# Kernel tuning notes

Measured on AMD Instinct MI355X. Metric: run time of the kernel, lower is better.

Reference implementation:

```python
import jax, jax.numpy as jnp
import numpy as np

N_NODES = 100000
N_EDGES = 1600000
IN_C, HID_C, OUT_C = 128, 128, 128


def setup_inputs() -> dict:
    key = jax.random.key(0)
    k_x, k_e, k_w1, k_w2 = jax.random.split(key, 4)
    x = jax.random.normal(k_x, (N_NODES, IN_C), dtype=jnp.float32)
    edge_index = jax.random.randint(k_e, (2, N_EDGES), 0, N_NODES, dtype=jnp.int64)
    # Glorot-style init for GCNConv linear weights
    s1 = (6.0 / (IN_C + HID_C)) ** 0.5
    s2 = (6.0 / (HID_C + OUT_C)) ** 0.5
    W1 = jax.random.uniform(k_w1, (IN_C, HID_C), jnp.float32, -s1, s1)
    b1 = jnp.zeros((HID_C,), jnp.float32)
    W2 = jax.random.uniform(k_w2, (HID_C, OUT_C), jnp.float32, -s2, s2)
    b2 = jnp.zeros((OUT_C,), jnp.float32)
    return {"x": x, "edge_index": edge_index, "W1": W1, "b1": b1, "W2": W2, "b2": b2}


def gcn_conv(x, src, dst, W, b, num_nodes):
    # PyG GCNConv: linear transform, then sym-normalized aggregation with self-loops.
    h = x @ W                                   # [N, out]
    ones = jnp.ones_like(dst, dtype=h.dtype)
    # degree counts include the self-loop (+1)
    deg = jax.ops.segment_sum(ones, dst, num_segments=num_nodes) + 1.0
    inv_sqrt = jax.lax.rsqrt(deg)               # deg > 0 since self-loops
    coef = inv_sqrt[src] * inv_sqrt[dst]        # [E]
    msgs = h[src] * coef[:, None]               # [E, out] gather + scale
    agg = jax.ops.segment_sum(msgs, dst, num_segments=num_nodes)
    # self-loop contribution: coef = 1/deg for the (i,i) edge
    agg = agg + h * (inv_sqrt * inv_sqrt)[:, None]
    return agg + b


def reference(x, edge_index, W1, b1, W2, b2):
    src, dst = edge_index[0], edge_index[1]
    h = gcn_conv(x, src, dst, W1, b1, N_NODES)
    h = jax.nn.relu(h)
    out = gcn_conv(h, src, dst, W2, b2, N_NODES)
    return out
```

## Files before the change

### kernel.cpp

```cpp
#include <hip/hip_runtime.h>
#include <hip/hip_bf16.h>
#include <hip/hip_fp16.h>

#define N_NODES 100000
#define N_EDGES 1600000
#define C 128

typedef _Float16 half8 __attribute__((ext_vector_type(8)));
typedef _Float16 half4v __attribute__((ext_vector_type(4)));
typedef float f32x4 __attribute__((ext_vector_type(4)));

__global__ __launch_bounds__(256) void scan_block(const int* __restrict__ deg,
                                                  int* __restrict__ rowptr,
                                                  int* __restrict__ partial, int n) {
    __shared__ int s[256];
    int tid = threadIdx.x;
    int i = blockIdx.x * 256 + tid;
    int v = (i < n) ? deg[i] : 0;
    s[tid] = v;
    __syncthreads();
    for (int off = 1; off < 256; off <<= 1) {
        int t = (tid >= off) ? s[tid - off] : 0;
        __syncthreads();
        s[tid] += t;
        __syncthreads();
    }
    if (i < n) rowptr[i] = s[tid] - v;
    if (tid == 255) partial[blockIdx.x] = s[255];
}

__global__ __launch_bounds__(512) void scan_partial(int* __restrict__ partial, int n) {
    __shared__ int s[512];
    int tid = threadIdx.x;
    int v = (tid < n) ? partial[tid] : 0;
    s[tid] = v;
    __syncthreads();
    for (int off = 1; off < 512; off <<= 1) {
        int t = (tid >= off) ? s[tid - off] : 0;
        __syncthreads();
        s[tid] += t;
        __syncthreads();
    }
    if (tid < n) partial[tid] = s[tid] - v;
}

__global__ __launch_bounds__(256) void scan_finalize(int* __restrict__ rowptr,
                                                     const int* __restrict__ partial,
                                                     const int* __restrict__ deg,
                                                     float* __restrict__ isq,
                                                     int n, int E) {
    int i = blockIdx.x * 256 + threadIdx.x;
    if (i < n) {
        rowptr[i] += partial[blockIdx.x];
        isq[i] = rsqrtf((float)deg[i] + 1.0f);
    }
    if (i == 0) rowptr[n] = E;
}

__global__ __launch_bounds__(256) void fill_scatter(const int* __restrict__ src,
                                                    const int* __restrict__ dst,
                                                    const int* __restrict__ rank,
                                                    const int* __restrict__ rowptr,
                                                    const float* __restrict__ isq,
                                                    long long* __restrict__ edges, int E) {
    int i = blockIdx.x * 256 + threadIdx.x;
    if (i < E) {
        int d = dst[i];
        int s = src[i];
        int pos = rowptr[d] + rank[i];
        unsigned int cf = __float_as_uint(isq[s] * isq[d]);
        long long rec = (long long)(((unsigned long long)cf << 32) |
                                    (unsigned long long)(unsigned int)s);
        __builtin_nontemporal_store(rec, &edges[pos]);
    }
}

__global__ __launch_bounds__(256) void init_kernel(const float* __restrict__ W1,
                                                   const float* __restrict__ W2,
                                                   _Float16* __restrict__ W1s,
                                                   _Float16* __restrict__ W2s,
                                                   int* __restrict__ deg, int n) {
    if (blockIdx.x < 16) {
        int i = blockIdx.x * 256 + threadIdx.x;
        int which = i >> 11;
        int u = i & 2047;
        int lane = u & 63, l = lane & 15, q = lane >> 4;
        int ct = u >> 6, c = ct >> 3, t = ct & 7;
        const float* Wsrc = which ? W2 : W1;
        _Float16* Dst = which ? W2s : W1s;
        half8 v;
#pragma unroll
        for (int j = 0; j < 8; j++)
            v[j] = (_Float16)Wsrc[(c * 32 + q * 8 + j) * C + t * 16 + l];
        *(half8*)(Dst + (size_t)u * 8) = v;
    } else {
        int i = (blockIdx.x - 16) * 256 + threadIdx.x;
        if (i < n) deg[i] = 0;
    }
}

template <typename T>
__device__ __forceinline__ void gemm_body(const T* __restrict__ A,
                                          const _Float16* __restrict__ Wsw,
                                          _Float16* __restrict__ out, int n,
                                          int bid, int tid, _Float16* smem) {
    int lane = tid & 63;
    int w = tid >> 6;
    int m0 = bid * 64;

    if constexpr (sizeof(T) == 4) {
        const float4* A4 = (const float4*)A;
#pragma unroll
        for (int p = 0; p < 8; p++) {
            int idx = p * 256 + tid;
            int r = idx >> 5, f4 = idx & 31;
            int row = m0 + r; if (row >= n) row = n - 1;
            float4 v = A4[(size_t)row * 32 + f4];
            int kg = f4 >> 1, hi = f4 & 1;
            half4v hv = {(_Float16)v.x, (_Float16)v.y, (_Float16)v.z, (_Float16)v.w};
            *(half4v*)(smem + r * 128 + ((kg ^ (r & 15)) * 8) + hi * 4) = hv;
        }
    } else {
#pragma unroll
        for (int p = 0; p < 4; p++) {
            int idx = p * 256 + tid;
            int r = idx >> 4, kg = idx & 15;
            int row = m0 + r; if (row >= n) row = n - 1;
            half8 v = *(const half8*)(A + (size_t)row * C + kg * 8);
            *(half8*)(smem + r * 128 + ((kg ^ (r & 15)) * 8)) = v;
        }
    }
    __syncthreads();

    int l = lane & 15, q = lane >> 4;
    f32x4 acc[8] = {};

#pragma unroll
    for (int c = 0; c < 4; c++) {
        half8 af = *(const half8*)(smem + (w * 16 + l) * 128 + (((c * 4 + q) ^ l) * 8));
#pragma unroll
        for (int t = 0; t < 8; t++) {
            half8 bf = *(const half8*)(Wsw + (size_t)((c * 8 + t) * 64 + lane) * 8);
            acc[t] = __builtin_amdgcn_mfma_f32_16x16x32_f16(af, bf, acc[t], 0, 0, 0);
        }
    }

    __syncthreads();
    _Float16* cb = smem + w * 2176;
#pragma unroll
    for (int t = 0; t < 8; t++)
#pragma unroll
        for (int i = 0; i < 4; i++)
            cb[(q * 4 + i) * 136 + t * 16 + l] = (_Float16)acc[t][i];
    __syncthreads();
#pragma unroll
    for (int i = 0; i < 4; i++) {
        int r16 = i * 4 + q;
        int row = m0 + w * 16 + r16;
        if (row < n)
            *(half8*)(out + (size_t)row * C + l * 8) =
                *(const half8*)(cb + r16 * 136 + l * 8);
    }
}

template <typename T>
__global__ __launch_bounds__(256) void gemm_mfma(const T* __restrict__ A,
                                                 const _Float16* __restrict__ Wsw,
                                                 _Float16* __restrict__ out, int n) {
    __shared__ _Float16 smem[8704];
    gemm_body<T>(A, Wsw, out, n, blockIdx.x, threadIdx.x, smem);
}

__global__ __launch_bounds__(256) void fused_deg_gemm(const float* __restrict__ x,
                                                      const _Float16* __restrict__ W1s,
                                                      _Float16* __restrict__ h16, int n,
                                                      const int* __restrict__ dst,
                                                      int* __restrict__ deg,
                                                      int* __restrict__ rank, int E,
                                                      int nbG) {
    __shared__ _Float16 smem[8704];
    if ((int)blockIdx.x < nbG) {
        gemm_body<float>(x, W1s, h16, n, blockIdx.x, threadIdx.x, smem);
    } else {
        int i = (blockIdx.x - nbG) * 256 + threadIdx.x;
        if (i < E) rank[i] = atomicAdd(&deg[dst[i]], 1);
    }
}

template <bool RELU, typename OT>
__global__ __launch_bounds__(256) void aggregate(const _Float16* __restrict__ h,
                                                 const int* __restrict__ rowptr,
                                                 const long long* __restrict__ edges,
                                                 const float* __restrict__ isq,
                                                 const float* __restrict__ bias,
                                                 OT* __restrict__ out, int n) {
    int lane = threadIdx.x & 63;
    int wave = threadIdx.x >> 6;
    int node = blockIdx.x * 4 + wave;
    if (node >= n) return;

    int q   = lane >> 4;
    int l16 = lane & 15;
    int cb  = l16 * 8;

    int beg = rowptr[node];
    int end = rowptr[node + 1];

    float acc[8] = {};

    int j = beg + q;
    for (; j + 12 < end; j += 16) {
        unsigned long long e0 = (unsigned long long)edges[j];
        unsigned long long e1 = (unsigned long long)edges[j + 4];
        unsigned long long e2 = (unsigned long long)edges[j + 8];
        unsigned long long e3 = (unsigned long long)edges[j + 12];
        half8 h0 = *(const half8*)(h + (size_t)(unsigned int)e0 * C + cb);
        half8 h1 = *(const half8*)(h + (size_t)(unsigned int)e1 * C + cb);
        half8 h2 = *(const half8*)(h + (size_t)(unsigned int)e2 * C + cb);
        half8 h3 = *(const half8*)(h + (size_t)(unsigned int)e3 * C + cb);
        float c0 = __uint_as_float((unsigned int)(e0 >> 32));
        float c1 = __uint_as_float((unsigned int)(e1 >> 32));
        float c2 = __uint_as_float((unsigned int)(e2 >> 32));
        float c3 = __uint_as_float((unsigned int)(e3 >> 32));
#pragma unroll
        for (int k = 0; k < 8; k++) acc[k] += c0 * (float)h0[k];
#pragma unroll
        for (int k = 0; k < 8; k++) acc[k] += c1 * (float)h1[k];
#pragma unroll
        for (int k = 0; k < 8; k++) acc[k] += c2 * (float)h2[k];
#pragma unroll
        for (int k = 0; k < 8; k++) acc[k] += c3 * (float)h3[k];
    }
    for (; j < end; j += 4) {
        unsigned long long e = (unsigned long long)edges[j];
        half8 hv = *(const half8*)(h + (size_t)(unsigned int)e * C + cb);
        float cf = __uint_as_float((unsigned int)(e >> 32));
#pragma unroll
        for (int k = 0; k < 8; k++) acc[k] += cf * (float)hv[k];
    }

#pragma unroll
    for (int k = 0; k < 8; k++) {
        acc[k] += __shfl_xor(acc[k], 16, 64);
        acc[k] += __shfl_xor(acc[k], 32, 64);
    }

    if (q == 0) {
        float invd = isq[node];
        float sc = invd * invd;
        half8 hd = *(const half8*)(h + (size_t)node * C + cb);
        float4 bv0 = *(const float4*)(bias + cb);
        float4 bv1 = *(const float4*)(bias + cb + 4);
        float bb[8] = {bv0.x, bv0.y, bv0.z, bv0.w, bv1.x, bv1.y, bv1.z, bv1.w};
#pragma unroll
        for (int k = 0; k < 8; k++) {
            acc[k] += sc * (float)hd[k] + bb[k];
            if (RELU) acc[k] = fmaxf(acc[k], 0.f);
        }
        if constexpr (sizeof(OT) == 2) {
            half8 o;
#pragma unroll
            for (int k = 0; k < 8; k++) o[k] = (_Float16)acc[k];
            *(half8*)((_Float16*)out + (size_t)node * C + cb) = o;
        } else {
            float4 o0 = {acc[0], acc[1], acc[2], acc[3]};
            float4 o1 = {acc[4], acc[5], acc[6], acc[7]};
            *(float4*)((float*)out + (size_t)node * C + cb) = o0;
            *(float4*)((float*)out + (size_t)node * C + cb + 4) = o1;
        }
    }
}

extern "C" void kernel_launch(void* const* d_in, const int* in_sizes, int n_in,
                              void* d_out, int out_size, void* d_ws, size_t ws_size,
                              hipStream_t stream) {
    const float* x  = (const float*)d_in[0];
    const int* ei   = (const int*)d_in[1];
    const float* W1 = (const float*)d_in[2];
    const float* b1 = (const float*)d_in[3];
    const float* W2 = (const float*)d_in[4];
    const float* b2 = (const float*)d_in[5];
    float* out = (float*)d_out;

    const int N = N_NODES, E = N_EDGES;
    const int* src = ei;
    const int* dst = ei + E;

    char* ws = (char*)d_ws;
    size_t off = 0;
    auto alloc = [&](size_t bytes) {
        size_t o = off;
        off = (off + bytes + 255) & ~(size_t)255;
        return o;
    };
    _Float16* h16   = (_Float16*)(ws + alloc((size_t)N * C * 2));
    _Float16* hB16  = (_Float16*)(ws + alloc((size_t)N * C * 2));
    _Float16* W1s   = (_Float16*)(ws + alloc((size_t)C * C * 2));
    _Float16* W2s   = (_Float16*)(ws + alloc((size_t)C * C * 2));
    int*      deg   = (int*)     (ws + alloc((size_t)N * 4));
    float*    isq   = (float*)   (ws + alloc((size_t)N * 4));
    int*    rowptr  = (int*)     (ws + alloc((size_t)(N + 1) * 4));
    int*    rank    = (int*)     (ws + alloc((size_t)E * 4));
    int*    part    = (int*)     (ws + alloc((size_t)512 * 4));
    long long* edges = (long long*)(ws + alloc((size_t)E * 8));
    (void)ws_size; (void)n_in; (void)in_sizes; (void)out_size;

    const int nbN = (N + 255) / 256;
    const int nbE = (E + 255) / 256;
    const int nbG = (N + 63) / 64;

    init_kernel<<<16 + nbN, 256, 0, stream>>>(W1, W2, W1s, W2s, deg, N);

    fused_deg_gemm<<<nbG + nbE, 256, 0, stream>>>(x, W1s, h16, N, dst, deg, rank, E, nbG);

    scan_block<<<nbN, 256, 0, stream>>>(deg, rowptr, part, N);
    scan_partial<<<1, 512, 0, stream>>>(part, nbN);
    scan_finalize<<<nbN, 256, 0, stream>>>(rowptr, part, deg, isq, N, E);

    fill_scatter<<<nbE, 256, 0, stream>>>(src, dst, rank, rowptr, isq, edges, E);

    aggregate<true, _Float16><<<(N + 3) / 4, 256, 0, stream>>>(h16, rowptr, edges, isq, b1, hB16, N);

    gemm_mfma<_Float16><<<nbG, 256, 0, stream>>>(hB16, W2s, h16, N);

    aggregate<false, float><<<(N + 3) / 4, 256, 0, stream>>>(h16, rowptr, edges, isq, b2, out, N);
}
```

Measured before the change: 385.2 us.

## Replace global-atomic CSR build with two-level bucket sort using shared-memory atomics

The CSR construction drops per-edge global atomics on the degree array followed by a random scatter. It now does a two-pass bucket sort: per-chunk histograms over 128-node buckets, a global scan, a shared-atomic scatter into buckets fused with the first GEMM, then a per-bucket node sort that also produces rowptr and isq, and finally a coefficient fill. The goal is to cut global atomic contention and make the scatter writes more local. In exchange it adds an extra edge-buffer pass and more launches, and the order of edges within a node becomes nondeterministic, which changes floating-point summation order.

```diff
diff --git a/kernel.cpp b/kernel.cpp
--- a/kernel.cpp
+++ b/kernel.cpp
@@ -5,81 +5,21 @@
 #define N_NODES 100000
 #define N_EDGES 1600000
 #define C 128
+#define NB 782
+#define NC 256
+#define EPC (N_EDGES / NC)
 
 typedef _Float16 half8 __attribute__((ext_vector_type(8)));
 typedef _Float16 half4v __attribute__((ext_vector_type(4)));
 typedef float f32x4 __attribute__((ext_vector_type(4)));
 
-__global__ __launch_bounds__(256) void scan_block(const int* __restrict__ deg,
-                                                  int* __restrict__ rowptr,
-                                                  int* __restrict__ partial, int n) {
-    __shared__ int s[256];
-    int tid = threadIdx.x;
-    int i = blockIdx.x * 256 + tid;
-    int v = (i < n) ? deg[i] : 0;
-    s[tid] = v;
-    __syncthreads();
-    for (int off = 1; off < 256; off <<= 1) {
-        int t = (tid >= off) ? s[tid - off] : 0;
-        __syncthreads();
-        s[tid] += t;
-        __syncthreads();
-    }
-    if (i < n) rowptr[i] = s[tid] - v;
-    if (tid == 255) partial[blockIdx.x] = s[255];
-}
-
-__global__ __launch_bounds__(512) void scan_partial(int* __restrict__ partial, int n) {
-    __shared__ int s[512];
-    int tid = threadIdx.x;
-    int v = (tid < n) ? partial[tid] : 0;
-    s[tid] = v;
-    __syncthreads();
-    for (int off = 1; off < 512; off <<= 1) {
-        int t = (tid >= off) ? s[tid - off] : 0;
-        __syncthreads();
-        s[tid] += t;
-        __syncthreads();
-    }
-    if (tid < n) partial[tid] = s[tid] - v;
-}
-
-__global__ __launch_bounds__(256) void scan_finalize(int* __restrict__ rowptr,
-                                                     const int* __restrict__ partial,
-                                                     const int* __restrict__ deg,
-                                                     float* __restrict__ isq,
-                                                     int n, int E) {
-    int i = blockIdx.x * 256 + threadIdx.x;
-    if (i < n) {
-        rowptr[i] += partial[blockIdx.x];
-        isq[i] = rsqrtf((float)deg[i] + 1.0f);
-    }
-    if (i == 0) rowptr[n] = E;
-}
-
-__global__ __launch_bounds__(256) void fill_scatter(const int* __restrict__ src,
-                                                    const int* __restrict__ dst,
-                                                    const int* __restrict__ rank,
-                                                    const int* __restrict__ rowptr,
-                                                    const float* __restrict__ isq,
-                                                    long long* __restrict__ edges, int E) {
-    int i = blockIdx.x * 256 + threadIdx.x;
-    if (i < E) {
-        int d = dst[i];
-        int s = src[i];
-        int pos = rowptr[d] + rank[i];
-        unsigned int cf = __float_as_uint(isq[s] * isq[d]);
-        long long rec = (long long)(((unsigned long long)cf << 32) |
-                                    (unsigned long long)(unsigned int)s);
-        __builtin_nontemporal_store(rec, &edges[pos]);
-    }
-}
-
-__global__ __launch_bounds__(256) void init_kernel(const float* __restrict__ W1,
-                                                   const float* __restrict__ W2,
-                                                   _Float16* __restrict__ W1s,
-                                                   _Float16* __restrict__ W2s,
-                                                   int* __restrict__ deg, int n) {
+__global__ __launch_bounds__(256) void init_count(const float* __restrict__ W1,
+                                                  const float* __restrict__ W2,
+                                                  _Float16* __restrict__ W1s,
+                                                  _Float16* __restrict__ W2s,
+                                                  const int* __restrict__ dst,
+                                                  int* __restrict__ cnt) {
+    __shared__ int hist[NB];
     if (blockIdx.x < 16) {
         int i = blockIdx.x * 256 + threadIdx.x;
         int which = i >> 11;
@@ -94,9 +34,55 @@
             v[j] = (_Float16)Wsrc[(c * 32 + q * 8 + j) * C + t * 16 + l];
         *(half8*)(Dst + (size_t)u * 8) = v;
     } else {
-        int i = (blockIdx.x - 16) * 256 + threadIdx.x;
-        if (i < n) deg[i] = 0;
-    }
+        int c = blockIdx.x - 16;
+        int tid = threadIdx.x;
+        for (int b = tid; b < NB; b += 256) hist[b] = 0;
+        __syncthreads();
+        int base = c * EPC;
+        for (int i = tid; i < EPC; i += 256)
+            atomicAdd(&hist[dst[base + i] >> 7], 1);
+        __syncthreads();
+        for (int b = tid; b < NB; b += 256) cnt[b * NC + c] = hist[b];
+    }
+}
+
+__global__ __launch_bounds__(256) void scan_block2(int* __restrict__ a,
+                                                   int* __restrict__ partial, int n) {
+    __shared__ int s[256];
+    int tid = threadIdx.x;
+    int i = blockIdx.x * 256 + tid;
+    int v = (i < n) ? a[i] : 0;
+    s[tid] = v;
+    __syncthreads();
+    for (int off = 1; off < 256; off <<= 1) {
+        int t = (tid >= off) ? s[tid - off] : 0;
+        __syncthreads();
+        s[tid] += t;
+        __syncthreads();
+    }
+    if (i < n) a[i] = s[tid] - v;
+    if (tid == 255) partial[blockIdx.x] = s[255];
+}
+
+__global__ __launch_bounds__(1024) void scan_partial_1024(int* __restrict__ partial, int n) {
+    __shared__ int s[1024];
+    int tid = threadIdx.x;
+    int v = (tid < n) ? partial[tid] : 0;
+    s[tid] = v;
+    __syncthreads();
+    for (int off = 1; off < 1024; off <<= 1) {
+        int t = (tid >= off) ? s[tid - off] : 0;
+        __syncthreads();
+        s[tid] += t;
+        __syncthreads();
+    }
+    if (tid < n) partial[tid] = s[tid] - v;
+}
+
+__global__ __launch_bounds__(256) void scan_add(int* __restrict__ a,
+                                                const int* __restrict__ partial, int n) {
+    int i = blockIdx.x * 256 + threadIdx.x;
+    if (i < n) a[i] += partial[blockIdx.x];
 }
 
 template <typename T>
@@ -171,19 +157,98 @@
     gemm_body<T>(A, Wsw, out, n, blockIdx.x, threadIdx.x, smem);
 }
 
-__global__ __launch_bounds__(256) void fused_deg_gemm(const float* __restrict__ x,
-                                                      const _Float16* __restrict__ W1s,
-                                                      _Float16* __restrict__ h16, int n,
-                                                      const int* __restrict__ dst,
-                                                      int* __restrict__ deg,
-                                                      int* __restrict__ rank, int E,
-                                                      int nbG) {
+__global__ __launch_bounds__(256) void fused_gemm_scatter(const float* __restrict__ x,
+                                                          const _Float16* __restrict__ W1s,
+                                                          _Float16* __restrict__ h16, int n,
+                                                          const int* __restrict__ src,
+                                                          const int* __restrict__ dst,
+                                                          const int* __restrict__ S,
+                                                          long long* __restrict__ bsorted,
+                                                          int nbG) {
     __shared__ _Float16 smem[8704];
     if ((int)blockIdx.x < nbG) {
         gemm_body<float>(x, W1s, h16, n, blockIdx.x, threadIdx.x, smem);
     } else {
-        int i = (blockIdx.x - nbG) * 256 + threadIdx.x;
-        if (i < E) rank[i] = atomicAdd(&deg[dst[i]], 1);
+        int c = blockIdx.x - nbG;
+        int tid = threadIdx.x;
+        int* off = (int*)smem;
+        for (int b = tid; b < NB; b += 256) off[b] = S[b * NC + c];
+        __syncthreads();
+        int base = c * EPC;
+        for (int i = tid; i < EPC; i += 256) {
+            int s = src[base + i];
+            int d = dst[base + i];
+            int p = atomicAdd(&off[d >> 7], 1);
+            bsorted[p] = ((long long)(unsigned long long)(unsigned int)d << 32) |
+                         (unsigned int)s;
+        }
+    }
+}
+
+__global__ __launch_bounds__(256) void node_sort(const long long* __restrict__ bsorted,
+                                                 const int* __restrict__ S,
+                                                 long long* __restrict__ final2,
+                                                 int* __restrict__ rowptr,
+                                                 float* __restrict__ isq) {
+    __shared__ int hist[128];
+    __shared__ int sc[128];
+    __shared__ int off2[128];
+    __shared__ float iqb[128];
+    int b = blockIdx.x, tid = threadIdx.x;
+    int beg = S[b * NC];
+    int end = (b == NB - 1) ? N_EDGES : S[(b + 1) * NC];
+    if (tid < 128) hist[tid] = 0;
+    __syncthreads();
+    for (int i = beg + tid; i < end; i += 256) {
+        int d = (int)((unsigned long long)bsorted[i] >> 32);
+        atomicAdd(&hist[d & 127], 1);
+    }
+    __syncthreads();
+    if (tid < 128) sc[tid] = hist[tid];
+    __syncthreads();
+    for (int off = 1; off < 128; off <<= 1) {
+        int t = 0;
+        if (tid < 128 && tid >= off) t = sc[tid - off];
+        __syncthreads();
+        if (tid < 128) sc[tid] += t;
+        __syncthreads();
+    }
+    if (tid < 128) {
+        int node = b * 128 + tid;
+        int deg = hist[tid];
+        int start = beg + sc[tid] - deg;
+        off2[tid] = start;
+        if (node < N_NODES) {
+            rowptr[node] = start;
+            float iq = rsqrtf((float)deg + 1.0f);
+            isq[node] = iq;
+            iqb[tid] = iq;
+        }
+    }
+    if (b == 0 && tid == 0) rowptr[N_NODES] = N_EDGES;
+    __syncthreads();
+    for (int i = beg + tid; i < end; i += 256) {
+        long long rec = bsorted[i];
+        int d = (int)((unsigned long long)rec >> 32);
+        int li = d & 127;
+        int p = atomicAdd(&off2[li], 1);
+        final2[p] = ((long long)(unsigned long long)__float_as_uint(iqb[li]) << 32) |
+                    (unsigned int)(rec & 0xffffffffLL);
+    }
+}
+
+__global__ __launch_bounds__(256) void coef_fill(const long long* __restrict__ final2,
+                                                 const float* __restrict__ isq,
+                                                 long long* __restrict__ edges, int E) {
+    int i = blockIdx.x * 256 + threadIdx.x;
+    if (i < E) {
+        long long rec = final2[i];
+        int s = (int)(rec & 0xffffffffLL);
+        float iqd = __uint_as_float((unsigned int)((unsigned long long)rec >> 32));
+        float cf = isq[s] * iqd;
+        long long orec = ((long long)(unsigned long long)__float_as_uint(cf) << 32) |
+                         (unsigned int)s;
+        __builtin_nontemporal_store(orec, &edges[i]);
     }
 }
 
@@ -297,31 +362,35 @@
     _Float16* hB16  = (_Float16*)(ws + alloc((size_t)N * C * 2));
     _Float16* W1s   = (_Float16*)(ws + alloc((size_t)C * C * 2));
     _Float16* W2s   = (_Float16*)(ws + alloc((size_t)C * C * 2));
-    int*      deg   = (int*)     (ws + alloc((size_t)N * 4));
+    int*      cnt   = (int*)     (ws + alloc((size_t)NB * NC * 4));
+    int*      part  = (int*)     (ws + alloc((size_t)1024 * 4));
+    long long* ebuf1 = (long long*)(ws + alloc((size_t)E * 8));
+    long long* ebuf2 = (long long*)(ws + alloc((size_t)E * 8));
+    int*    rowptr  = (int*)     (ws + alloc((size_t)(N + 1) * 4));
     float*    isq   = (float*)   (ws + alloc((size_t)N * 4));
-    int*    rowptr  = (int*)     (ws + alloc((size_t)(N + 1) * 4));
-    int*    rank    = (int*)     (ws + alloc((size_t)E * 4));
-    int*    part    = (int*)     (ws + alloc((size_t)512 * 4));
-    long long* edges = (long long*)(ws + alloc((size_t)E * 8));
     (void)ws_size; (void)n_in; (void)in_sizes; (void)out_size;
 
-    const int nbN = (N + 255) / 256;
+    const int nbG = (N + 63) / 64;
+    const int nS  = NB * NC;
+    const int nbS = nS / 256;
     const int nbE = (E + 255) / 256;
-    const int nbG = (N + 63) / 64;
-
-    init_kernel<<<16 + nbN, 256, 0, stream>>>(W1, W2, W1s, W2s, deg, N);
-
-    fused_deg_gemm<<<nbG + nbE, 256, 0, stream>>>(x, W1s, h16, N, dst, deg, rank, E, nbG);
-
-    scan_block<<<nbN, 256, 0, stream>>>(deg, rowptr, part, N);
-    scan_partial<<<1, 512, 0, stream>>>(part, nbN);
-    scan_finalize<<<nbN, 256, 0, stream>>>(rowptr, part, deg, isq, N, E);
-
-    fill_scatter<<<nbE, 256, 0, stream>>>(src, dst, rank, rowptr, isq, edges, E);
-
-    aggregate<true, _Float16><<<(N + 3) / 4, 256, 0, stream>>>(h16, rowptr, edges, isq, b1, hB16, N);
+
+    init_count<<<16 + NC, 256, 0, stream>>>(W1, W2, W1s, W2s, dst, cnt);
+
+    scan_block2<<<nbS, 256, 0, stream>>>(cnt, part, nS);
+    scan_partial_1024<<<1, 1024, 0, stream>>>(part, nbS);
+    scan_add<<<nbS, 256, 0, stream>>>(cnt, part, nS);
+
+    fused_gemm_scatter<<<nbG + NC, 256, 0, stream>>>(x, W1s, h16, N, src, dst, cnt,
+                                                     ebuf1, nbG);
+
+    node_sort<<<NB, 256, 0, stream>>>(ebuf1, cnt, ebuf2, rowptr, isq);
+
+    coef_fill<<<nbE, 256, 0, stream>>>(ebuf2, isq, ebuf1, E);
+
+    aggregate<true, _Float16><<<(N + 3) / 4, 256, 0, stream>>>(h16, rowptr, ebuf1, isq, b1, hB16, N);
 
     gemm_mfma<_Float16><<<nbG, 256, 0, stream>>>(hB16, W2s, h16, N);
 
-    aggregate<false, float><<<(N + 3) / 4, 256, 0, stream>>>(h16, rowptr, edges, isq, b2, out, N);
-}
+    aggregate<false, float><<<(N + 3) / 4, 256, 0, stream>>>(h16, rowptr, ebuf1, isq, b2, out, N);
+}
```

Result: faster. 339.0 us (-12.0%).
